# Kernel optimization log

Measured on AMD Instinct MI355X. Metric: run time of the kernel, lower is better.

Reference implementation:

```python
import jax, jax.numpy as jnp
import numpy as np

N, DEG = 20000, 16          # nodes, fixed neighbor-list length
H, C, D, IN = 4, 16, 128, 256  # cluster_heads, num_centroids, hidden_dim, input_dim
NEG_SLOPE = 0.2


def setup_inputs() -> dict:
    key = jax.random.key(0)
    ks = jax.random.split(key, 12)
    s_in = 1.0 / np.sqrt(IN)
    s_h = 1.0 / np.sqrt(D)
    inp = {
        "x_node": jax.random.normal(ks[0], (N, IN), dtype=jnp.float32),
        "adj": jax.random.randint(ks[1], (N, DEG), 0, N, dtype=jnp.int32),
        "epoch": 1,
        # linear layers (torch convention: W [out, in])
        "W1": jax.random.uniform(ks[2], (D, IN), jnp.float32, -s_in, s_in),
        "b1": jax.random.uniform(ks[3], (D,), jnp.float32, -s_in, s_in),
        "W2": jax.random.uniform(ks[4], (D, D), jnp.float32, -s_h, s_h),
        "b2": jax.random.uniform(ks[5], (D,), jnp.float32, -s_h, s_h),
        "W21": jax.random.uniform(ks[6], (D, D), jnp.float32, -s_h, s_h),
        "b21": jax.random.uniform(ks[7], (D,), jnp.float32, -s_h, s_h),
        # centroids: 2*rand-1, shape [H, C*D]
        "centroids": 2.0 * jax.random.uniform(ks[8], (H, C * D), dtype=jnp.float32) - 1.0,
        # headConv: xavier_uniform gain=1.414 on [H, 1]
        "headConv": jax.random.uniform(ks[9], (H, 1), jnp.float32,
                                       -1.414 * np.sqrt(6.0 / (H + 1)),
                                       1.414 * np.sqrt(6.0 / (H + 1))),
    }
    return inp


def _leaky(x):
    return jnp.where(x >= 0, x, NEG_SLOPE * x)


def _cluster_block(h, adj, centroids, headConv):
    # h: [N, D]; adj: [N, deg]; centroids: [H, C*D]; headConv: [H, 1]
    cent = centroids.reshape(H, C, D)
    # squared L2 distance dist[h,c,n] = ||x_n - cent_hc||^2 (norm expansion,
    # avoids the [H,C,N,D] broadcast the torch code materializes)
    hn2 = jnp.sum(h * h, axis=-1)                      # [N]
    cn2 = jnp.sum(cent * cent, axis=-1)                # [H, C]
    cross = jnp.einsum('hcd,nd->hcn', cent, h)         # [H, C, N]
    dist = cn2[..., None] + hn2[None, None, :] - 2.0 * cross
    # nu=1: q = (1 + dist)^-1
    q = 1.0 / (1.0 + dist)                             # [H, C, N]
    # gather neighbor scores per node and normalize over the edge dim
    qn = q[:, :, adj]                                  # [H, C, N, deg]
    qn = qn / jnp.sum(qn, axis=3, keepdims=True)
    # combine heads with headConv, then softmax over edges per centroid
    w = jnp.einsum('hcne,h->nce', qn, headConv[:, 0])  # [N, C, deg]
    w = jax.nn.softmax(w, axis=2)
    # weighted aggregation of neighbor features
    new_feat = jnp.einsum('nce,ned->ncd', w, h[adj])   # [N, C, D]
    return new_feat


def reference(x_node, adj, epoch, W1, b1, W2, b2, W21, b21, centroids, headConv):
    # eval mode: dropout is identity
    x = _leaky(x_node @ W1.T + b1)
    h_prime = _leaky(x @ W2.T + b2)                    # [N, D]
    new_feat = _cluster_block(h_prime, adj, centroids, headConv)
    new_feat = _leaky(new_feat @ W21.T + b21)          # [N, C, D]
    return (h_prime, new_feat)
```

## Files before the change

### kernel.cpp

```cpp
#include <hip/hip_runtime.h>
#include <cstdint>
#include <cstddef>

#define NEG_SLOPE 0.2f

typedef __attribute__((ext_vector_type(8))) short bf16x8;
typedef __attribute__((ext_vector_type(8))) unsigned short u16x8;
typedef __attribute__((ext_vector_type(4))) float f32x4;
typedef __attribute__((ext_vector_type(2))) float f32x2;

__device__ __forceinline__ float leaky_f(float x) { return x >= 0.f ? x : NEG_SLOPE * x; }

__device__ __forceinline__ unsigned short f2bf(float f) {
    union { float f; uint32_t u; } v; v.f = f;
    return (unsigned short)((v.u + 0x7fffu + ((v.u >> 16) & 1u)) >> 16);
}
__device__ __forceinline__ float bf2f(unsigned short u) {
    union { uint32_t u; float f; } v; v.u = ((uint32_t)u) << 16; return v.f;
}
__device__ __forceinline__ float bfhi(uint32_t w) {
    union { uint32_t u; float f; } v; v.u = w & 0xffff0000u; return v.f;
}
__device__ __forceinline__ float bflo(uint32_t w) {
    union { uint32_t u; float f; } v; v.u = w << 16; return v.f;
}
__device__ __forceinline__ u16x8 cvt8(float4 a, float4 b) {
    u16x8 o;
    o[0] = f2bf(a.x); o[1] = f2bf(a.y); o[2] = f2bf(a.z); o[3] = f2bf(a.w);
    o[4] = f2bf(b.x); o[5] = f2bf(b.y); o[6] = f2bf(b.z); o[7] = f2bf(b.w);
    return o;
}

#if __has_builtin(__builtin_elementwise_fma)
__device__ __forceinline__ f32x2 fma2(f32x2 a, f32x2 b, f32x2 c) {
    return __builtin_elementwise_fma(a, b, c);
}
#else
__device__ __forceinline__ f32x2 fma2(f32x2 a, f32x2 b, f32x2 c) {
    f32x2 r; r[0] = fmaf(a[0], b[0], c[0]); r[1] = fmaf(a[1], b[1], c[1]); return r;
}
#endif

__device__ __forceinline__ float xor32_add(float v) {
    float y = v;
    asm volatile("v_permlane32_swap_b32 %0, %1" : "+v"(y), "+v"(v));
    return v + y;
}

__global__ __launch_bounds__(256)
void pack_kernel(const float* __restrict__ x_node, const float* __restrict__ W1,
                 const float* __restrict__ W2, const float* __restrict__ W21,
                 const float* __restrict__ cent,
                 unsigned short* __restrict__ xb, unsigned short* __restrict__ pw1,
                 unsigned short* __restrict__ pw2, unsigned short* __restrict__ pw3,
                 float* __restrict__ cn2g, int N)
{
    const int bid = blockIdx.x, tid = threadIdx.x;
    if (bid < 36) {
        const int sub = tid >> 6, lane = tid & 63, g = bid * 4 + sub;
        const int l15 = lane & 15, l4 = lane >> 4;
        const float* src; unsigned short* dst;
        if (g < 64) {
            int step = g >> 3, f = g & 7;
            src = W1 + (size_t)(f * 16 + l15) * 256 + step * 32 + l4 * 8;
            dst = pw1 + ((size_t)(step * 8 + f) * 64 + lane) * 8;
        } else if (g < 96) {
            int gg = g - 64, step = gg >> 3, f = gg & 7;
            src = W2 + (size_t)(f * 16 + l15) * 128 + step * 32 + l4 * 8;
            dst = pw2 + ((size_t)(step * 8 + f) * 64 + lane) * 8;
        } else {
            int gg = g - 96, step = gg / 12, f = gg % 12;
            int brow = f * 16 + l15;
            const float* base = (brow < 128) ? (W21 + (size_t)brow * 128)
                                             : (cent + (size_t)(brow - 128) * 128);
            src = base + step * 32 + l4 * 8;
            dst = pw3 + ((size_t)(step * 12 + f) * 64 + lane) * 8;
        }
        float4 a = *reinterpret_cast<const float4*>(src);
        float4 b = *reinterpret_cast<const float4*>(src + 4);
        *reinterpret_cast<u16x8*>(dst) = cvt8(a, b);
    } else if (bid == 36) {
        int r = tid >> 2, c0 = (tid & 3) * 32;
        const float* cr = cent + (size_t)r * 128 + c0;
        float s = 0.f;
#pragma unroll
        for (int q = 0; q < 8; q++) {
            float4 v = *reinterpret_cast<const float4*>(cr + q * 4);
            s += v.x * v.x + v.y * v.y + v.z * v.z + v.w * v.w;
        }
        s += __shfl_xor(s, 1); s += __shfl_xor(s, 2);
        if ((tid & 3) == 0) cn2g[r] = s;
    } else {
        size_t base = (size_t)(bid - 37) * 4096 + (size_t)tid * 16;
        float4 v0 = *reinterpret_cast<const float4*>(x_node + base);
        float4 v1 = *reinterpret_cast<const float4*>(x_node + base + 4);
        float4 v2 = *reinterpret_cast<const float4*>(x_node + base + 8);
        float4 v3 = *reinterpret_cast<const float4*>(x_node + base + 12);
        *reinterpret_cast<u16x8*>(xb + base)     = cvt8(v0, v1);
        *reinterpret_cast<u16x8*>(xb + base + 8) = cvt8(v2, v3);
    }
}

__global__ __launch_bounds__(256)
void fused_gemms(const unsigned short* __restrict__ xb,
                 const unsigned short* __restrict__ pw1, const unsigned short* __restrict__ pw2,
                 const unsigned short* __restrict__ pw3,
                 const float* __restrict__ b1, const float* __restrict__ b2,
                 const float* __restrict__ cn2g,
                 float* __restrict__ h_out, unsigned short* __restrict__ hWb,
                 unsigned short* __restrict__ qtb, int N)
{
    __shared__ __align__(16) short Xs[32 * 136];
    __shared__ float hn2s[4][32];

    const int tid = threadIdx.x, wave = tid >> 6, lane = tid & 63;
    const int l15 = lane & 15, l4 = lane >> 4;
    const int rowBlk = blockIdx.x * 32;

    f32x4 a00{0.f,0.f,0.f,0.f}, a01{0.f,0.f,0.f,0.f}, a10{0.f,0.f,0.f,0.f}, a11{0.f,0.f,0.f,0.f};
    {
        const unsigned short* ap0 = xb + (size_t)(rowBlk + l15) * 256 + l4 * 8;
        const unsigned short* ap1 = ap0 + 16 * 256;
        const unsigned short* bp = pw1 + (size_t)(wave * 2) * 512 + lane * 8;
#pragma unroll
        for (int k = 0; k < 8; k++) {
            bf16x8 af0 = *reinterpret_cast<const bf16x8*>(ap0 + k * 32);
            bf16x8 af1 = *reinterpret_cast<const bf16x8*>(ap1 + k * 32);
            bf16x8 bf0 = *reinterpret_cast<const bf16x8*>(bp + (size_t)k * 8 * 512);
            bf16x8 bf1 = *reinterpret_cast<const bf16x8*>(bp + (size_t)k * 8 * 512 + 512);
            a00 = __builtin_amdgcn_mfma_f32_16x16x32_bf16(af0, bf0, a00, 0, 0, 0);
            a01 = __builtin_amdgcn_mfma_f32_16x16x32_bf16(af0, bf1, a01, 0, 0, 0);
            a10 = __builtin_amdgcn_mfma_f32_16x16x32_bf16(af1, bf0, a10, 0, 0, 0);
            a11 = __builtin_amdgcn_mfma_f32_16x16x32_bf16(af1, bf1, a11, 0, 0, 0);
        }
        float bia = b1[wave * 32 + l15], bib = b1[wave * 32 + 16 + l15];
#pragma unroll
        for (int j = 0; j < 4; j++) {
            int r0 = l4 * 4 + j;
            Xs[r0 * 136 + wave * 32 + l15]             = (short)f2bf(leaky_f(a00[j] + bia));
            Xs[r0 * 136 + wave * 32 + 16 + l15]        = (short)f2bf(leaky_f(a01[j] + bib));
            Xs[(r0 + 16) * 136 + wave * 32 + l15]      = (short)f2bf(leaky_f(a10[j] + bia));
            Xs[(r0 + 16) * 136 + wave * 32 + 16 + l15] = (short)f2bf(leaky_f(a11[j] + bib));
        }
    }
    __syncthreads();

    a00 = f32x4{0.f,0.f,0.f,0.f}; a01 = f32x4{0.f,0.f,0.f,0.f};
    a10 = f32x4{0.f,0.f,0.f,0.f}; a11 = f32x4{0.f,0.f,0.f,0.f};
    const short* xp0 = &Xs[l15 * 136 + l4 * 8];
    const short* xp1 = &Xs[(16 + l15) * 136 + l4 * 8];
    {
        const unsigned short* bp = pw2 + (size_t)(wave * 2) * 512 + lane * 8;
#pragma unroll
        for (int k = 0; k < 4; k++) {
            bf16x8 af0 = *reinterpret_cast<const bf16x8*>(xp0 + k * 32);
            bf16x8 af1 = *reinterpret_cast<const bf16x8*>(xp1 + k * 32);
            bf16x8 bf0 = *reinterpret_cast<const bf16x8*>(bp + (size_t)k * 8 * 512);
            bf16x8 bf1 = *reinterpret_cast<const bf16x8*>(bp + (size_t)k * 8 * 512 + 512);
            a00 = __builtin_amdgcn_mfma_f32_16x16x32_bf16(af0, bf0, a00, 0, 0, 0);
            a01 = __builtin_amdgcn_mfma_f32_16x16x32_bf16(af0, bf1, a01, 0, 0, 0);
            a10 = __builtin_amdgcn_mfma_f32_16x16x32_bf16(af1, bf0, a10, 0, 0, 0);
            a11 = __builtin_amdgcn_mfma_f32_16x16x32_bf16(af1, bf1, a11, 0, 0, 0);
        }
    }
    float hv00[4], hv01[4], hv10[4], hv11[4], pn0[4], pn1[4];
    {
        float bia = b2[wave * 32 + l15], bib = b2[wave * 32 + 16 + l15];
#pragma unroll
        for (int j = 0; j < 4; j++) {
            hv00[j] = leaky_f(a00[j] + bia);
            hv01[j] = leaky_f(a01[j] + bib);
            hv10[j] = leaky_f(a10[j] + bia);
            hv11[j] = leaky_f(a11[j] + bib);
            float s0 = hv00[j] * hv00[j] + hv01[j] * hv01[j];
            s0 += __shfl_xor(s0, 1); s0 += __shfl_xor(s0, 2);
            s0 += __shfl_xor(s0, 4); s0 += __shfl_xor(s0, 8);
            pn0[j] = s0;
            float s1 = hv10[j] * hv10[j] + hv11[j] * hv11[j];
            s1 += __shfl_xor(s1, 1); s1 += __shfl_xor(s1, 2);
            s1 += __shfl_xor(s1, 4); s1 += __shfl_xor(s1, 8);
            pn1[j] = s1;
        }
    }
    __syncthreads();

#pragma unroll
    for (int j = 0; j < 4; j++) {
        int r0 = l4 * 4 + j;
        Xs[r0 * 136 + wave * 32 + l15]             = (short)f2bf(hv00[j]);
        Xs[r0 * 136 + wave * 32 + 16 + l15]        = (short)f2bf(hv01[j]);
        Xs[(r0 + 16) * 136 + wave * 32 + l15]      = (short)f2bf(hv10[j]);
        Xs[(r0 + 16) * 136 + wave * 32 + 16 + l15] = (short)f2bf(hv11[j]);
        __builtin_nontemporal_store(hv00[j], &h_out[(size_t)(rowBlk + r0) * 128 + wave * 32 + l15]);
        __builtin_nontemporal_store(hv01[j], &h_out[(size_t)(rowBlk + r0) * 128 + wave * 32 + 16 + l15]);
        __builtin_nontemporal_store(hv10[j], &h_out[(size_t)(rowBlk + 16 + r0) * 128 + wave * 32 + l15]);
        __builtin_nontemporal_store(hv11[j], &h_out[(size_t)(rowBlk + 16 + r0) * 128 + wave * 32 + 16 + l15]);
        if (l15 == 0) { hn2s[wave][r0] = pn0[j]; hn2s[wave][16 + r0] = pn1[j]; }
    }
    __syncthreads();

    f32x4 c00{0.f,0.f,0.f,0.f}, c01{0.f,0.f,0.f,0.f}, c02{0.f,0.f,0.f,0.f};
    f32x4 c10{0.f,0.f,0.f,0.f}, c11{0.f,0.f,0.f,0.f}, c12{0.f,0.f,0.f,0.f};
    {
        const unsigned short* bp = pw3 + (size_t)(wave * 3) * 512 + lane * 8;
#pragma unroll
        for (int k = 0; k < 4; k++) {
            bf16x8 af0 = *reinterpret_cast<const bf16x8*>(xp0 + k * 32);
            bf16x8 af1 = *reinterpret_cast<const bf16x8*>(xp1 + k * 32);
            bf16x8 bf0 = *reinterpret_cast<const bf16x8*>(bp + (size_t)k * 12 * 512);
            bf16x8 bf1 = *reinterpret_cast<const bf16x8*>(bp + (size_t)k * 12 * 512 + 512);
            bf16x8 bf2 = *reinterpret_cast<const bf16x8*>(bp + (size_t)k * 12 * 512 + 1024);
            c00 = __builtin_amdgcn_mfma_f32_16x16x32_bf16(af0, bf0, c00, 0, 0, 0);
            c01 = __builtin_amdgcn_mfma_f32_16x16x32_bf16(af0, bf1, c01, 0, 0, 0);
            c02 = __builtin_amdgcn_mfma_f32_16x16x32_bf16(af0, bf2, c02, 0, 0, 0);
            c10 = __builtin_amdgcn_mfma_f32_16x16x32_bf16(af1, bf0, c10, 0, 0, 0);
            c11 = __builtin_amdgcn_mfma_f32_16x16x32_bf16(af1, bf1, c11, 0, 0, 0);
            c12 = __builtin_amdgcn_mfma_f32_16x16x32_bf16(af1, bf2, c12, 0, 0, 0);
        }
    }
    {
        float hn2r0[4], hn2r1[4];
#pragma unroll
        for (int j = 0; j < 4; j++) {
            int r0 = l4 * 4 + j;
            hn2r0[j] = hn2s[0][r0] + hn2s[1][r0] + hn2s[2][r0] + hn2s[3][r0];
            hn2r1[j] = hn2s[0][16 + r0] + hn2s[1][16 + r0] + hn2s[2][16 + r0] + hn2s[3][16 + r0];
        }
        f32x4 av0[3] = {c00, c01, c02};
        f32x4 av1[3] = {c10, c11, c12};
#pragma unroll
        for (int ff = 0; ff < 3; ff++) {
            int col = wave * 48 + ff * 16 + l15;
            if (col < 128) {
#pragma unroll
                for (int j = 0; j < 4; j++) {
                    int gr0 = rowBlk + l4 * 4 + j;
                    hWb[(size_t)gr0 * 128 + col]        = f2bf(av0[ff][j]);
                    hWb[(size_t)(gr0 + 16) * 128 + col] = f2bf(av1[ff][j]);
                }
            } else {
                int c2 = col - 128;
                float cn2v = cn2g[c2];
#pragma unroll
                for (int j = 0; j < 4; j++) {
                    int gr0 = rowBlk + l4 * 4 + j;
                    float q0 = 1.f / (1.f + cn2v + hn2r0[j] - 2.f * av0[ff][j]);
                    float q1 = 1.f / (1.f + cn2v + hn2r1[j] - 2.f * av1[ff][j]);
                    qtb[(size_t)gr0 * 64 + c2]        = f2bf(q0);
                    qtb[(size_t)(gr0 + 16) * 64 + c2] = f2bf(q1);
                }
            }
        }
    }
}

struct PerWaveU {
    union {
        unsigned short qs[1024];
        float wbuf[16][16];
    };
};

__global__ __launch_bounds__(256)
void agg_kernel(const int* __restrict__ adj, const unsigned short* __restrict__ qtb,
                const unsigned short* __restrict__ hWb, const float* __restrict__ b21,
                const float* __restrict__ headConv, float* __restrict__ out1)
{
    __shared__ __align__(16) unsigned short hs[4][16 * 128];
    __shared__ __align__(16) PerWaveU upw[4];

    const int wv = threadIdx.x >> 6, lane = threadIdx.x & 63;
    const int eg = lane >> 4, l15 = lane & 15;
    const int n = blockIdx.x * 4 + wv;

    const int myadj = adj[n * 16 + l15];

#pragma unroll
    for (int i = 0; i < 2; i++) {
        int row = i * 8 + (lane >> 3);
        int nb = __shfl(myadj, row);
        *reinterpret_cast<u16x8*>(&upw[wv].qs[i * 512 + lane * 8]) =
            *reinterpret_cast<const u16x8*>(qtb + (size_t)nb * 64 + (lane & 7) * 8);
    }
#pragma unroll
    for (int i = 0; i < 4; i++) {
        int row = i * 4 + eg;
        int nb = __shfl(myadj, row);
        *reinterpret_cast<u16x8*>(&hs[wv][i * 512 + lane * 8]) =
            *reinterpret_cast<const u16x8*>(hWb + (size_t)nb * 128 + l15 * 8);
    }

    {
        float qv[16];
        float s = 0.f;
#pragma unroll
        for (int e = 0; e < 16; e++) { qv[e] = bf2f(upw[wv].qs[e * 64 + lane]); s += qv[e]; }
        float rs = 1.f / s;
        float conv = headConv[eg];
        float ex[4] = {0.f, 0.f, 0.f, 0.f};
#pragma unroll
        for (int e = 0; e < 16; e++) {
            float v = conv * qv[e] * rs;
            v += __shfl_xor(v, 16);
            v = xor32_add(v);
            float evv = __expf(v);
            bool mine = (eg == (e >> 2));
            ex[e & 3] = mine ? evv : ex[e & 3];
        }
        float ps = ex[0] + ex[1] + ex[2] + ex[3];
        ps += __shfl_xor(ps, 16);
        ps = xor32_add(ps);
        float inv = 1.f / ps;
#pragma unroll
        for (int j = 0; j < 4; j++) upw[wv].wbuf[eg * 4 + j][l15] = ex[j] * inv;
    }

    {
        const int d0 = l15 * 4;
        float bvf[8];
        *reinterpret_cast<float4*>(bvf)     = *reinterpret_cast<const float4*>(b21 + d0);
        *reinterpret_cast<float4*>(bvf + 4) = *reinterpret_cast<const float4*>(b21 + d0 + 64);
        f32x2 acc2[4][4];
#pragma unroll
        for (int jc = 0; jc < 4; jc++) {
            acc2[jc][0] = f32x2{bvf[0], bvf[1]};
            acc2[jc][1] = f32x2{bvf[2], bvf[3]};
            acc2[jc][2] = f32x2{bvf[4], bvf[5]};
            acc2[jc][3] = f32x2{bvf[6], bvf[7]};
        }

#pragma unroll
        for (int e = 0; e < 16; e++) {
            uint2 wlo = *reinterpret_cast<const uint2*>(&hs[wv][e * 128 + d0]);
            uint2 whi = *reinterpret_cast<const uint2*>(&hs[wv][e * 128 + 64 + d0]);
            float w4[4];
            *reinterpret_cast<float4*>(w4) =
                *reinterpret_cast<const float4*>(&upw[wv].wbuf[e][eg * 4]);
            f32x2 hv2[4];
            hv2[0] = f32x2{bflo(wlo.x), bfhi(wlo.x)};
            hv2[1] = f32x2{bflo(wlo.y), bfhi(wlo.y)};
            hv2[2] = f32x2{bflo(whi.x), bfhi(whi.x)};
            hv2[3] = f32x2{bflo(whi.y), bfhi(whi.y)};
#pragma unroll
            for (int jc = 0; jc < 4; jc++) {
                f32x2 w2 = f32x2{w4[jc], w4[jc]};
#pragma unroll
                for (int q = 0; q < 4; q++)
                    acc2[jc][q] = fma2(w2, hv2[q], acc2[jc][q]);
            }
        }

#pragma unroll
        for (int jc = 0; jc < 4; jc++) {
            f32x4 lo, hi;
            lo[0] = leaky_f(acc2[jc][0][0]); lo[1] = leaky_f(acc2[jc][0][1]);
            lo[2] = leaky_f(acc2[jc][1][0]); lo[3] = leaky_f(acc2[jc][1][1]);
            hi[0] = leaky_f(acc2[jc][2][0]); hi[1] = leaky_f(acc2[jc][2][1]);
            hi[2] = leaky_f(acc2[jc][3][0]); hi[3] = leaky_f(acc2[jc][3][1]);
            float* dst = out1 + ((size_t)(n * 16 + eg * 4 + jc)) * 128;
            __builtin_nontemporal_store(lo, reinterpret_cast<f32x4*>(dst + d0));
            __builtin_nontemporal_store(hi, reinterpret_cast<f32x4*>(dst + d0 + 64));
        }
    }
}

extern "C" void kernel_launch(void* const* d_in, const int* in_sizes, int n_in,
                              void* d_out, int out_size, void* d_ws, size_t ws_size,
                              hipStream_t stream)
{
    const float* x_node   = (const float*)d_in[0];
    const int*   adj      = (const int*)  d_in[1];
    const float* W1       = (const float*)d_in[3];
    const float* b1       = (const float*)d_in[4];
    const float* W2       = (const float*)d_in[5];
    const float* b2       = (const float*)d_in[6];
    const float* W21      = (const float*)d_in[7];
    const float* b21      = (const float*)d_in[8];
    const float* cent     = (const float*)d_in[9];
    const float* headConv = (const float*)d_in[10];

    const int N = in_sizes[0] / 256;

    float* h    = (float*)d_out;
    float* out1 = h + (size_t)N * 128;

    unsigned short* xb  = (unsigned short*)d_ws;
    unsigned short* hWb = xb  + (size_t)N * 256;
    unsigned short* qtb = hWb + (size_t)N * 128;
    unsigned short* pw1 = qtb + (size_t)N * 64;
    unsigned short* pw2 = pw1 + 32768;
    unsigned short* pw3 = pw2 + 16384;
    float*          cn2g = (float*)(pw3 + 24576);

    const int xblocks = (N * 256) / 4096;

    pack_kernel<<<37 + xblocks, 256, 0, stream>>>(x_node, W1, W2, W21, cent,
                                                  xb, pw1, pw2, pw3, cn2g, N);
    fused_gemms<<<N / 32, 256, 0, stream>>>(xb, pw1, pw2, pw3, b1, b2, cn2g,
                                            h, hWb, qtb, N);
    agg_kernel<<<N / 4, 256, 0, stream>>>(adj, qtb, hWb, b21, headConv, out1);
}
```

Before: 64.06 us.

## Split each node's aggregation across two waves by feature half

The aggregation kernel now assigns two waves per node, each handling 64 of the 128 output feature columns, and the grid doubles to N/2 blocks. Each wave loads only its half of the neighbor hidden rows into a smaller shared buffer and keeps half as many accumulators, which lowers register and LDS pressure and raises parallelism. In exchange, the neighbor score gather, normalization and softmax are computed redundantly by both waves of a node.

```diff
diff --git a/kernel.cpp b/kernel.cpp
--- a/kernel.cpp
+++ b/kernel.cpp
@@ -266,14 +266,15 @@
                 const unsigned short* __restrict__ hWb, const float* __restrict__ b21,
                 const float* __restrict__ headConv, float* __restrict__ out1)
 {
-    __shared__ __align__(16) unsigned short hs[4][16 * 128];
+    __shared__ __align__(16) unsigned short hs[4][16 * 64];
     __shared__ __align__(16) PerWaveU upw[4];
 
     const int wv = threadIdx.x >> 6, lane = threadIdx.x & 63;
     const int eg = lane >> 4, l15 = lane & 15;
-    const int n = blockIdx.x * 4 + wv;
-
-    const int myadj = adj[n * 16 + l15];
+    const int n = blockIdx.x * 2 + (wv >> 1);
+    const int dh = (wv & 1) * 64;
+
+    const int myadj = adj[(size_t)n * 16 + l15];
 
 #pragma unroll
     for (int i = 0; i < 2; i++) {
@@ -281,13 +282,8 @@
         int nb = __shfl(myadj, row);
         *reinterpret_cast<u16x8*>(&upw[wv].qs[i * 512 + lane * 8]) =
             *reinterpret_cast<const u16x8*>(qtb + (size_t)nb * 64 + (lane & 7) * 8);
-    }
-#pragma unroll
-    for (int i = 0; i < 4; i++) {
-        int row = i * 4 + eg;
-        int nb = __shfl(myadj, row);
         *reinterpret_cast<u16x8*>(&hs[wv][i * 512 + lane * 8]) =
-            *reinterpret_cast<const u16x8*>(hWb + (size_t)nb * 128 + l15 * 8);
+            *reinterpret_cast<const u16x8*>(hWb + (size_t)nb * 128 + dh + (lane & 7) * 8);
     }
 
     {
@@ -317,49 +313,39 @@
 
     {
         const int d0 = l15 * 4;
-        float bvf[8];
-        *reinterpret_cast<float4*>(bvf)     = *reinterpret_cast<const float4*>(b21 + d0);
-        *reinterpret_cast<float4*>(bvf + 4) = *reinterpret_cast<const float4*>(b21 + d0 + 64);
-        f32x2 acc2[4][4];
+        float bvf[4];
+        *reinterpret_cast<float4*>(bvf) = *reinterpret_cast<const float4*>(b21 + dh + d0);
+        f32x2 acc2[4][2];
 #pragma unroll
         for (int jc = 0; jc < 4; jc++) {
             acc2[jc][0] = f32x2{bvf[0], bvf[1]};
             acc2[jc][1] = f32x2{bvf[2], bvf[3]};
-            acc2[jc][2] = f32x2{bvf[4], bvf[5]};
-            acc2[jc][3] = f32x2{bvf[6], bvf[7]};
         }
 
 #pragma unroll
         for (int e = 0; e < 16; e++) {
-            uint2 wlo = *reinterpret_cast<const uint2*>(&hs[wv][e * 128 + d0]);
-            uint2 whi = *reinterpret_cast<const uint2*>(&hs[wv][e * 128 + 64 + d0]);
+            uint2 hraw = *reinterpret_cast<const uint2*>(&hs[wv][e * 64 + d0]);
             float w4[4];
             *reinterpret_cast<float4*>(w4) =
                 *reinterpret_cast<const float4*>(&upw[wv].wbuf[e][eg * 4]);
-            f32x2 hv2[4];
-            hv2[0] = f32x2{bflo(wlo.x), bfhi(wlo.x)};
-            hv2[1] = f32x2{bflo(wlo.y), bfhi(wlo.y)};
-            hv2[2] = f32x2{bflo(whi.x), bfhi(whi.x)};
-            hv2[3] = f32x2{bflo(whi.y), bfhi(whi.y)};
+            f32x2 hv2[2];
+            hv2[0] = f32x2{bflo(hraw.x), bfhi(hraw.x)};
+            hv2[1] = f32x2{bflo(hraw.y), bfhi(hraw.y)};
 #pragma unroll
             for (int jc = 0; jc < 4; jc++) {
                 f32x2 w2 = f32x2{w4[jc], w4[jc]};
-#pragma unroll
-                for (int q = 0; q < 4; q++)
-                    acc2[jc][q] = fma2(w2, hv2[q], acc2[jc][q]);
+                acc2[jc][0] = fma2(w2, hv2[0], acc2[jc][0]);
+                acc2[jc][1] = fma2(w2, hv2[1], acc2[jc][1]);
             }
         }
 
 #pragma unroll
         for (int jc = 0; jc < 4; jc++) {
-            f32x4 lo, hi;
-            lo[0] = leaky_f(acc2[jc][0][0]); lo[1] = leaky_f(acc2[jc][0][1]);
-            lo[2] = leaky_f(acc2[jc][1][0]); lo[3] = leaky_f(acc2[jc][1][1]);
-            hi[0] = leaky_f(acc2[jc][2][0]); hi[1] = leaky_f(acc2[jc][2][1]);
-            hi[2] = leaky_f(acc2[jc][3][0]); hi[3] = leaky_f(acc2[jc][3][1]);
-            float* dst = out1 + ((size_t)(n * 16 + eg * 4 + jc)) * 128;
-            __builtin_nontemporal_store(lo, reinterpret_cast<f32x4*>(dst + d0));
-            __builtin_nontemporal_store(hi, reinterpret_cast<f32x4*>(dst + d0 + 64));
+            f32x4 o;
+            o[0] = leaky_f(acc2[jc][0][0]); o[1] = leaky_f(acc2[jc][0][1]);
+            o[2] = leaky_f(acc2[jc][1][0]); o[3] = leaky_f(acc2[jc][1][1]);
+            float* dst = out1 + ((size_t)(n * 16 + eg * 4 + jc)) * 128 + dh;
+            __builtin_nontemporal_store(o, reinterpret_cast<f32x4*>(dst + d0));
         }
     }
 }
@@ -398,5 +384,5 @@
                                                   xb, pw1, pw2, pw3, cn2g, N);
     fused_gemms<<<N / 32, 256, 0, stream>>>(xb, pw1, pw2, pw3, b1, b2, cn2g,
                                             h, hWb, qtb, N);
-    agg_kernel<<<N / 4, 256, 0, stream>>>(adj, qtb, hWb, b21, headConv, out1);
-}
+    agg_kernel<<<N / 2, 256, 0, stream>>>(adj, qtb, hWb, b21, headConv, out1);
+}
```

Result: slower. 67.22 us (+4.9%).
